# Optimization experiments

Hardware: AMD Instinct MI355X
Metric: run time of the kernel (lower is better)

Reference implementation:

```python
import jax, jax.numpy as jnp
import numpy as np

N_GRAPHS = 256
GRADES = jnp.array([0, 1, 1, 1, 2, 2, 2, 3])      # blade -> grade for Cl(3,0): [1,e1,e2,e3,e12,e13,e23,e123]
G_ONEHOT = jnp.eye(4)[GRADES]                      # (8,4) blade->grade one-hot
NUM_RBF, CUTOFF, NEG_SLOPE = 20, 10.0, 0.2
HID, HEADS, HD, LAYERS = 64, 4, 16, 4
EPS_LN = 1e-6


def _mv_linear_sub(x, w, b):
    # MVLinear with per-grade weights. x:(N,I,8), w:(4,O,I), b:(O,) added to scalar blade.
    wb = w[GRADES]                                 # (8,O,I)
    out = jnp.einsum('nib,boi->nob', x, wb)
    return out.at[..., 0].add(b)


def _gat_layer(h, src, dst, edge_scalar, pw, pb, asrc, adst, wsrc, wdst):
    N = h.shape[0]
    z = _mv_linear_sub(h, pw, pb).reshape(N, HEADS, HD, 8)
    # fold per-grade importance weights into per-blade contraction vectors
    a_s = asrc * wsrc[:, GRADES][:, None, :]       # (H,C,8)
    a_d = adst * wdst[:, GRADES][:, None, :]
    s_src = jnp.einsum('nhcb,hcb->nh', z, a_s)
    s_dst = jnp.einsum('nhcb,hcb->nh', z, a_d)
    e = jax.nn.leaky_relu(s_src[src] + s_dst[dst] + edge_scalar, NEG_SLOPE)  # (E,H)
    e_max = jax.ops.segment_max(e, dst, num_segments=N)
    alpha = jnp.exp(e - e_max[dst])
    a_sum = jax.ops.segment_sum(alpha, dst, num_segments=N)
    alpha = alpha / (a_sum[dst] + 1e-16)
    out = jax.ops.segment_sum(z[src] * alpha[:, :, None, None], dst, num_segments=N)
    return out.reshape(N, HEADS * HD, 8)


def _mv_silu(x, a, b):
    # x:(N,C,8); a,b:(C,4). Gate by scalar part (grade 0) and per-grade squared magnitudes.
    qg = jnp.einsum('ncb,bg->ncg', x * x, G_ONEHOT)                 # (N,C,4) mag2 per grade
    norms = jnp.concatenate([x[..., :1], qg[..., 1:]], axis=-1)     # (N,C,4)
    gate = jax.nn.sigmoid(a * norms + b)[..., GRADES]               # (N,C,8)
    return gate * x


def _mv_layernorm(x, a):
    n = jnp.sqrt(jnp.sum(x * x, axis=-1))                           # (N,C)
    n = jnp.mean(n, axis=1, keepdims=True) + EPS_LN                 # (N,1)
    return a[None, :, None] * x / n[..., None]


def _forward(floats, z, edge_index, batch):
    (pos, atom_w, inw, inb, ew1, eb1, ew2, eb2,
     proj_w, proj_b, a_src, a_dst, w_src, w_dst,
     ln_a, silu_a, silu_b, ppw, ppb, pw1, pb1, pw2, pb2) = floats
    src, dst = edge_index[0], edge_index[1]
    N = pos.shape[0]

    # RBF edge features -> per-head scalar bias
    d2 = jnp.sum((pos[src] - pos[dst]) ** 2, axis=-1)
    dist = jnp.where(d2 > 0, jnp.sqrt(jnp.where(d2 > 0, d2, 1.0)), 0.0)
    centers = jnp.linspace(0.0, CUTOFF, NUM_RBF)
    width = CUTOFF / (NUM_RBF - 1)
    rbf = jnp.exp(-0.5 * ((dist[:, None] - centers) / width) ** 2)  # (E,20)
    edge_scalar = jax.nn.silu(rbf @ ew1.T + eb1) @ ew2.T + eb2      # (E,H)

    # node multivector embedding: scalars from atom embedding, grade-1 from centered positions
    h_sca = jnp.zeros((N, HID, 8), dtype=pos.dtype).at[..., 0].set(atom_w[z])
    cnt = jax.ops.segment_sum(jnp.ones((N,), pos.dtype), batch, num_segments=N_GRAPHS)
    pos_mean = jax.ops.segment_sum(pos, batch, num_segments=N_GRAPHS) / jnp.maximum(cnt, 1.0)[:, None]
    pos_c = pos - pos_mean[batch]
    h_vec = jnp.zeros((N, 1, 8), dtype=pos.dtype).at[:, 0, 1:4].set(pos_c)
    h = jnp.concatenate([h_sca, h_vec], axis=1)                     # (N,HID+1,8)
    h = jnp.einsum('nib,oi->nob', h, inw).at[..., 0].add(inb)       # input_proj, subspaces=False

    for l in range(LAYERS):
        h_res = h
        h = _gat_layer(h, src, dst, edge_scalar, proj_w[l], proj_b[l],
                       a_src[l], a_dst[l], w_src[l], w_dst[l])
        h = _mv_silu(h, silu_a[l], silu_b[l])
        h = h + h_res
        h = _mv_layernorm(h, ln_a[l])

    h = _mv_linear_sub(h, ppw, ppb)[..., 0]                         # (N,HID) scalar blade
    g = jax.ops.segment_sum(h, batch, num_segments=N_GRAPHS)        # 'add' readout -> (B,HID)
    out = jax.nn.silu(g @ pw1.T + pb1) @ pw2.T + pb2                # (B,1)
    return out[:, 0]


def setup_inputs() -> dict:
    key = jax.random.key(0)
    ks = jax.random.split(key, 24)
    N, E, B = 20000, 320000, N_GRAPHS
    rn = lambda k, shape, s=0.1: jax.random.normal(k, shape, jnp.float32) * s
    return dict(
        pos=jax.random.normal(ks[0], (N, 3), jnp.float32) * 3.0,
        z=jax.random.randint(ks[1], (N,), 0, 100),
        edge_index=jax.random.randint(ks[2], (2, E), 0, N),
        batch=jnp.sort(jax.random.randint(ks[3], (N,), 0, B)),
        atom_embed_w=rn(ks[4], (100, HID)),
        inproj_w=rn(ks[5], (HID, HID + 1)),
        inproj_b=rn(ks[6], (HID,)),
        edge_w1=rn(ks[7], (HID, NUM_RBF)),
        edge_b1=rn(ks[8], (HID,)),
        edge_w2=rn(ks[9], (HEADS, HID)),
        edge_b2=rn(ks[10], (HEADS,)),
        proj_w=rn(ks[11], (LAYERS, 4, HID, HID)),
        proj_b=rn(ks[12], (LAYERS, HID)),
        a_src=rn(ks[13], (LAYERS, HEADS, HD, 8)),
        a_dst=rn(ks[14], (LAYERS, HEADS, HD, 8)),
        w_src=jnp.ones((LAYERS, HEADS, 4), jnp.float32),
        w_dst=jnp.ones((LAYERS, HEADS, 4), jnp.float32),
        ln_a=jnp.ones((LAYERS, HID), jnp.float32),
        silu_a=jnp.ones((LAYERS, HID, 4), jnp.float32),
        silu_b=jnp.zeros((LAYERS, HID, 4), jnp.float32),
        prepool_w=rn(ks[15], (4, HID, HID)),
        prepool_b=rn(ks[16], (HID,)),
        post_w1=rn(ks[17], (HID, HID)),
        post_b1=rn(ks[18], (HID,)),
        post_w2=rn(ks[19], (1, HID)),
        post_b2=rn(ks[20], (1,)),
    )


def reference(pos, z, edge_index, batch, atom_embed_w, inproj_w, inproj_b,
              edge_w1, edge_b1, edge_w2, edge_b2, proj_w, proj_b,
              a_src, a_dst, w_src, w_dst, ln_a, silu_a, silu_b,
              prepool_w, prepool_b, post_w1, post_b1, post_w2, post_b2):
    floats = (pos, atom_embed_w, inproj_w, inproj_b, edge_w1, edge_b1, edge_w2, edge_b2,
              proj_w, proj_b, a_src, a_dst, w_src, w_dst,
              ln_a, silu_a, silu_b, prepool_w, prepool_b, post_w1, post_b1, post_w2, post_b2)
    return _forward(floats, z, edge_index, batch)
```

## Files before the change

kernel.cpp:

```cpp
#include <hip/hip_runtime.h>
#include <hip/hip_bf16.h>
#include <math.h>

#define HID 64
#define HEADS 4
#define LAYERS 4
#define NRBF 20
#define NG 256
#define CB 512
#define HSTRIDE 68
#define CAPB 64
#define TABN 8192
#define NATOM 100

typedef __attribute__((ext_vector_type(8))) short short8;
typedef __attribute__((ext_vector_type(4))) float floatx4;

__device__ __forceinline__ int gradeOf(int b){ return (b==0)?0:((b<4)?1:((b<7)?2:3)); }
__device__ __forceinline__ unsigned short f2bf(float f){
    __hip_bfloat16 h = __float2bfloat16(f);
    return *(unsigned short*)&h;
}
__device__ __forceinline__ float bflo(int u){ return __uint_as_float(((unsigned)u)<<16); }
__device__ __forceinline__ float bfhi(int u){ return __uint_as_float(((unsigned)u)&0xFFFF0000u); }
__device__ __forceinline__ int packbf2(float a, float b){
    return (int)f2bf(a) | ((int)f2bf(b)<<16);
}

struct P {
    const float *pos; const int *zidx; const int *ei; const int *batch;
    const float *atom_w, *inproj_w, *inproj_b, *ew1, *eb1, *ew2, *eb2;
    const float *proj_w, *proj_b, *a_src, *a_dst, *w_src, *w_dst;
    const float *ln_a, *silu_a, *silu_b, *ppw, *ppb, *pw1, *pb1, *pw2, *pb2;
    float *out;
    int *counts; float *possum; float *pcnt; float *gbuf;
    int *bucket;
    int *escb;
    float *tab;
    unsigned short *WTbf; float *ppw0T; float *w1T; float *sbf;
    float *embT;
    unsigned short *hb;
    unsigned short *zA; unsigned short *zB;
    float *ssA; float *sdA; float *ssB; float *sdB;
    int N, E, Mtiles;
};

__global__ __launch_bounds__(256) void k1_kernel(P p){
    const int PREP_TOTAL = LAYERS*4*64*64 + 2*HID*HID + 2*LAYERS*HEADS;
    const int CP = (PREP_TOTAL+255)/256;
    const int CG = NG/4;
    const int CT = (TABN+1+3)/4;
    int bid = blockIdx.x, t = threadIdx.x;
    if (bid < CP){
        int idx = bid*256 + t;
        const int szW = LAYERS*4*64*64;
        const int e2 = szW + HID*HID;
        const int e3 = e2 + HID*HID;
        if (idx < szW){
            p.WTbf[idx] = f2bf(p.proj_w[idx]);
        } else if (idx < e2){
            int r = idx - szW; int i = r/HID, o = r%HID;
            p.ppw0T[r] = p.ppw[o*HID + i];
        } else if (idx < e3){
            int r = idx - e2; int i = r/HID, o = r%HID;
            p.w1T[r] = p.pw1[o*HID + i];
        } else if (idx < e3 + 2*LAYERS*HEADS){
            int r = idx - e3;
            int hh = r & 3; int type = (r>>2)&1; int l = r>>3;
            const float* a = type ? p.a_dst : p.a_src;
            const float* w = type ? p.w_dst : p.w_src;
            float wh = w[l*16 + hh*4 + 0];
            float s = 0.f;
            for (int c=0;c<16;c++)
                s += a[l*512 + (hh*16+c)*8 + 0] * wh * p.proj_b[l*64 + hh*16 + c];
            p.sbf[r] = s;
        }
    } else if (bid < CP+CG){
        int wv = t>>6, lane = t&63;
        int g = (bid-CP)*4 + wv;
        int lo = 0, hi = p.N;
        while (lo < hi){ int mid = (lo+hi)>>1; if (p.batch[mid] < g) lo = mid+1; else hi = mid; }
        int s0 = lo;
        hi = p.N;
        while (lo < hi){ int mid = (lo+hi)>>1; if (p.batch[mid] < g+1) lo = mid+1; else hi = mid; }
        int s1 = lo;
        float sx=0.f, sy=0.f, sz=0.f;
        for (int i=s0+lane; i<s1; i+=64){
            sx += p.pos[i*3+0]; sy += p.pos[i*3+1]; sz += p.pos[i*3+2];
        }
        #pragma unroll
        for (int off=1; off<64; off<<=1){
            sx += __shfl_xor(sx,off,64);
            sy += __shfl_xor(sy,off,64);
            sz += __shfl_xor(sz,off,64);
        }
        if (lane==0){
            p.possum[g*3+0]=sx; p.possum[g*3+1]=sy; p.possum[g*3+2]=sz;
            p.pcnt[g] = (float)(s1-s0);
        }
    } else if (bid < CP+CG+CT){
        int wv = t>>6, lane = t&63;
        int i = (bid-CP-CG)*4 + wv;
        if (i > TABN) return;
        float d = (float)i * (16.0f/TABN);
        float t0 = d * (19.0f/10.0f);
        float hv = p.eb1[lane];
        #pragma unroll
        for (int k=0;k<NRBF;k++){
            float a = t0 - (float)k;
            hv += __expf(-0.5f*a*a) * p.ew1[lane*NRBF+k];
        }
        float act = hv/(1.0f+__expf(-hv));
        float p0 = act*p.ew2[0*HID+lane];
        float p1 = act*p.ew2[1*HID+lane];
        float p2 = act*p.ew2[2*HID+lane];
        float p3 = act*p.ew2[3*HID+lane];
        #pragma unroll
        for (int off=1; off<64; off<<=1){
            p0 += __shfl_xor(p0,off,64);
            p1 += __shfl_xor(p1,off,64);
            p2 += __shfl_xor(p2,off,64);
            p3 += __shfl_xor(p3,off,64);
        }
        if (lane==0){
            *(float4*)&p.tab[(size_t)i*4] = make_float4(p0+p.eb2[0], p1+p.eb2[1],
                                                        p2+p.eb2[2], p3+p.eb2[3]);
        }
    } else {
        int wv = t>>6, lane = t&63;
        int za = (bid-CP-CG-CT)*4 + wv;
        if (za >= NATOM) return;
        float accv = p.inproj_b[lane];
        for (int i=0;i<HID;i++)
            accv += p.atom_w[(size_t)za*HID + i] * p.inproj_w[lane*65 + i];
        p.embT[(size_t)za*HID + lane] = accv;
    }
}

__device__ __forceinline__ void proj_core(const P& p, int pl, int n0, int nt, int lane,
        const short8* afr, bool rows16,
        unsigned short* zout, float* ssout, float* sdout){
    const unsigned short* WTl = p.WTbf + (size_t)pl*4*64*64;
    const float* pbl = p.proj_b + pl*HID;
    const float* a_src_l = p.a_src + pl*512;
    const float* a_dst_l = p.a_dst + pl*512;
    const float* w_src_l = p.w_src + pl*16;
    const float* w_dst_l = p.w_dst + pl*16;
    const float* sb_l = p.sbf + pl*8;
    int m = lane&15, quad = lane>>4;
    int o = nt*16 + m;
    float cs[4][2][4];
    float pss[4], psd[4];
    #pragma unroll
    for (int r=0;r<4;r++){ pss[r]=0.f; psd[r]=0.f; }
    #pragma unroll
    for (int bp=0; bp<4; bp++){
        const int b0 = 2*bp, b1 = b0+1;
        const int g0 = gradeOf(b0), g1 = gradeOf(b1);
        const short8 w00 = *(const short8*)(WTl + (g0*64 + o)*64 + quad*8);
        const short8 w01 = *(const short8*)(WTl + (g0*64 + o)*64 + 32 + quad*8);
        short8 w10, w11;
        if (g1==g0){ w10 = w00; w11 = w01; }
        else {
            w10 = *(const short8*)(WTl + (g1*64 + o)*64 + quad*8);
            w11 = *(const short8*)(WTl + (g1*64 + o)*64 + 32 + quad*8);
        }
        floatx4 c0 = {0.f,0.f,0.f,0.f}, c1 = {0.f,0.f,0.f,0.f};
        c0 = __builtin_amdgcn_mfma_f32_16x16x32_bf16(afr[4*bp+0], w00, c0, 0,0,0);
        c0 = __builtin_amdgcn_mfma_f32_16x16x32_bf16(afr[4*bp+1], w01, c0, 0,0,0);
        c1 = __builtin_amdgcn_mfma_f32_16x16x32_bf16(afr[4*bp+2], w10, c1, 0,0,0);
        c1 = __builtin_amdgcn_mfma_f32_16x16x32_bf16(afr[4*bp+3], w11, c1, 0,0,0);
        float as0 = a_src_l[o*8+b0]*w_src_l[nt*4+g0];
        float as1 = a_src_l[o*8+b1]*w_src_l[nt*4+g1];
        float ad0 = a_dst_l[o*8+b0]*w_dst_l[nt*4+g0];
        float ad1 = a_dst_l[o*8+b1]*w_dst_l[nt*4+g1];
        float bias0 = (bp==0) ? pbl[o] : 0.0f;
        #pragma unroll
        for (int r=0;r<4;r++){
            float v0 = c0[r], v1 = c1[r];
            pss[r] += v0*as0 + v1*as1;
            psd[r] += v0*ad0 + v1*ad1;
            cs[bp][0][r] = v0 + bias0;
            cs[bp][1][r] = v1;
        }
    }
    #pragma unroll
    for (int r=0;r<4;r++){
        int row = quad*4 + r;
        bool rowok = rows16 ? true : (quad==0);
        int nn = n0 + (rows16 ? row : r);
        if (rowok && nn < p.N){
            unsigned short pk[8];
            #pragma unroll
            for (int bp=0;bp<4;bp++){
                pk[2*bp]   = f2bf(cs[bp][0][r]);
                pk[2*bp+1] = f2bf(cs[bp][1][r]);
            }
            *(int4*)(zout + (size_t)nn*CB + o*8) = *(int4*)pk;
        }
    }
    #pragma unroll
    for (int r=0;r<4;r++){
        float vs = pss[r], vd = psd[r];
        #pragma unroll
        for (int off=1; off<16; off<<=1){
            vs += __shfl_xor(vs, off, 64);
            vd += __shfl_xor(vd, off, 64);
        }
        int row = quad*4 + r;
        bool rowok = rows16 ? true : (quad==0);
        int nn = n0 + (rows16 ? row : r);
        if (m==0 && rowok && nn<p.N){
            ssout[nn*4+nt] = vs + sb_l[nt];
            sdout[nn*4+nt] = vd + sb_l[4+nt];
        }
    }
}

__global__ __launch_bounds__(256) void k2_kernel(P p){
    __shared__ unsigned short hAl[8*16*HSTRIDE];
    int t = threadIdx.x, wv = t>>6, lane = t&63;
    if ((int)blockIdx.x >= p.Mtiles){
        int e = ((int)blockIdx.x - p.Mtiles)*256 + t;
        if (e >= p.E) return;
        int s = p.ei[e], d = p.ei[p.E+e];
        float dx = p.pos[s*3+0]-p.pos[d*3+0];
        float dy = p.pos[s*3+1]-p.pos[d*3+1];
        float dz = p.pos[s*3+2]-p.pos[d*3+2];
        float dist = sqrtf(dx*dx+dy*dy+dz*dz);
        float idxf = fminf(dist * ((float)TABN/16.0f), (float)(TABN-1));
        int i0 = (int)idxf;
        float fr = idxf - (float)i0;
        float4 f0 = *(const float4*)&p.tab[(size_t)i0*4];
        float4 f1 = *(const float4*)&p.tab[(size_t)(i0+1)*4];
        int slot = atomicAdd(&p.counts[d],1);
        if (slot < CAPB){
            p.bucket[(size_t)d*CAPB + slot] = s;
            int2 epk = make_int2(
                packbf2(f0.x + (f1.x-f0.x)*fr, f0.y + (f1.y-f0.y)*fr),
                packbf2(f0.z + (f1.z-f0.z)*fr, f0.w + (f1.w-f0.w)*fr));
            *(int2*)&p.escb[((size_t)d*CAPB + slot)*2] = epk;
        }
        return;
    }
    int n0 = blockIdx.x*16;
    float wvv = p.inproj_w[lane*65 + 64];
    for (int k=0;k<4;k++){
        int m = wv*4 + k;
        int n = n0 + m;
        if (n < p.N){
            int zn = p.zidx[n];
            float acc = p.embT[(size_t)zn*HID + lane];
            int g = p.batch[n];
            float cm = p.pcnt[g]; cm = cm>1.0f?cm:1.0f;
            float px = p.pos[n*3+0]-p.possum[g*3+0]/cm;
            float py = p.pos[n*3+1]-p.possum[g*3+1]/cm;
            float pz = p.pos[n*3+2]-p.possum[g*3+2]/cm;
            unsigned short pk[8];
            pk[0]=f2bf(acc); pk[1]=f2bf(wvv*px); pk[2]=f2bf(wvv*py); pk[3]=f2bf(wvv*pz);
            pk[4]=0; pk[5]=0; pk[6]=0; pk[7]=0;
            *(int4*)(p.hb + (size_t)n*CB + lane*8) = *(int4*)pk;
            #pragma unroll
            for (int b=0;b<8;b++) hAl[(b*16+m)*HSTRIDE + lane] = pk[b];
        } else {
            #pragma unroll
            for (int b=0;b<8;b++) hAl[(b*16+m)*HSTRIDE + lane] = 0;
        }
    }
    __syncthreads();
    int m = lane&15, quad = lane>>4;
    short8 afr[16];
    #pragma unroll
    for (int bp=0;bp<4;bp++){
        int b0=2*bp, b1=b0+1;
        afr[4*bp+0] = *(const short8*)(hAl + (b0*16+m)*HSTRIDE + quad*8);
        afr[4*bp+1] = *(const short8*)(hAl + (b0*16+m)*HSTRIDE + 32 + quad*8);
        afr[4*bp+2] = *(const short8*)(hAl + (b1*16+m)*HSTRIDE + quad*8);
        afr[4*bp+3] = *(const short8*)(hAl + (b1*16+m)*HSTRIDE + 32 + quad*8);
    }
    proj_core(p, 0, n0, wv, lane, afr, true, p.zA, p.ssA, p.sdA);
}

__device__ __forceinline__ void fmab8(const float* lwv, int h_id, int J,
                                      const int4* zv, float* acc, float& dn){
    #pragma unroll
    for (int i=0;i<8;i++){
        float w = lwv[(J+i)*4 + h_id];
        acc[0] += w*bflo(zv[i].x); acc[1] += w*bfhi(zv[i].x);
        acc[2] += w*bflo(zv[i].y); acc[3] += w*bfhi(zv[i].y);
        acc[4] += w*bflo(zv[i].z); acc[5] += w*bfhi(zv[i].z);
        acc[6] += w*bflo(zv[i].w); acc[7] += w*bfhi(zv[i].w);
        dn += w;
    }
}

__global__ __launch_bounds__(256) void agg_kernel(P p, int l,
        const unsigned short* __restrict__ zin, const float* __restrict__ ssin,
        const float* __restrict__ sdin, int last){
    __shared__ float lw[4][256];
    int wv = threadIdx.x>>6, lane = threadIdx.x&63;
    int n = blockIdx.x*4 + wv;
    if (n >= p.N) return;
    float* lwv = lw[wv];
    int4 hres = *((const int4*)(p.hb + (size_t)n*CB) + lane);
    float4 sdl = *(const float4*)&sdin[n*4];
    int deg = min(p.counts[n], CAPB);
    int h_id = lane>>4;
    const int* bs = p.bucket + (size_t)n*CAPB;
    int s = 0;
    float l0=-1e30f,l1=-1e30f,l2=-1e30f,l3=-1e30f;
    if (lane < deg){
        s = bs[lane];
        int2 ev = *((const int2*)p.escb + ((size_t)n*CAPB + lane));
        float4 sv  = *(const float4*)&ssin[s*4];
        l0 = sv.x+sdl.x+bflo(ev.x); l0=(l0>=0.f)?l0:0.2f*l0;
        l1 = sv.y+sdl.y+bfhi(ev.x); l1=(l1>=0.f)?l1:0.2f*l1;
        l2 = sv.z+sdl.z+bflo(ev.y); l2=(l2>=0.f)?l2:0.2f*l2;
        l3 = sv.w+sdl.w+bfhi(ev.y); l3=(l3>=0.f)?l3:0.2f*l3;
    }
    int bc = (deg+7)>>3;
    int4 zv[8];
    if (bc>0){
        #pragma unroll
        for (int i=0;i<8;i++){
            int sb = __builtin_amdgcn_readlane(s, i);
            zv[i] = *((const int4*)(zin + (size_t)(unsigned)sb*CB) + lane);
        }
    }
    float m0=l0,m1=l1,m2=l2,m3=l3;
    #pragma unroll
    for (int off=1; off<64; off<<=1){
        m0=fmaxf(m0,__shfl_xor(m0,off,64));
        m1=fmaxf(m1,__shfl_xor(m1,off,64));
        m2=fmaxf(m2,__shfl_xor(m2,off,64));
        m3=fmaxf(m3,__shfl_xor(m3,off,64));
    }
    *(float4*)&lwv[lane*4] = make_float4(__expf(l0-m0),__expf(l1-m1),
                                         __expf(l2-m2),__expf(l3-m3));
    float acc[8];
    #pragma unroll
    for (int k=0;k<8;k++) acc[k]=0.f;
    float dn = 0.f;
    if (bc>0) fmab8(lwv, h_id, 0, zv, acc, dn);
    for (int j=8; j<bc*8; j+=8){
        #pragma unroll
        for (int i=0;i<8;i++){
            int sb = __builtin_amdgcn_readlane(s, j+i);
            zv[i] = *((const int4*)(zin + (size_t)(unsigned)sb*CB) + lane);
        }
        fmab8(lwv, h_id, j, zv, acc, dn);
    }
    float inv = 1.0f/(dn + 1e-16f);
    float x[8];
    #pragma unroll
    for (int k=0;k<8;k++) x[k] = acc[k]*inv;
    const float* silu_a_l = p.silu_a + l*HID*4;
    const float* silu_b_l = p.silu_b + l*HID*4;
    float4 sa = *(const float4*)&silu_a_l[lane*4];
    float4 sb = *(const float4*)&silu_b_l[lane*4];
    float n1 = x[1]*x[1]+x[2]*x[2]+x[3]*x[3];
    float n2 = x[4]*x[4]+x[5]*x[5]+x[6]*x[6];
    float n3 = x[7]*x[7];
    float g0 = 1.0f/(1.0f+__expf(-(sa.x*x[0]+sb.x)));
    float g1 = 1.0f/(1.0f+__expf(-(sa.y*n1+sb.y)));
    float g2 = 1.0f/(1.0f+__expf(-(sa.z*n2+sb.z)));
    float g3 = 1.0f/(1.0f+__expf(-(sa.w*n3+sb.w)));
    float val[8];
    val[0]=g0*x[0]+bflo(hres.x); val[1]=g1*x[1]+bfhi(hres.x);
    val[2]=g1*x[2]+bflo(hres.y); val[3]=g1*x[3]+bfhi(hres.y);
    val[4]=g2*x[4]+bflo(hres.z); val[5]=g2*x[5]+bfhi(hres.z);
    val[6]=g2*x[6]+bflo(hres.w); val[7]=g3*x[7]+bfhi(hres.w);
    float ssq=0.f;
    #pragma unroll
    for (int k=0;k<8;k++) ssq += val[k]*val[k];
    float nr = sqrtf(ssq);
    #pragma unroll
    for (int off=1; off<64; off<<=1) nr += __shfl_xor(nr, off, 64);
    float mean = nr*(1.0f/64.0f) + 1e-6f;
    float scale = p.ln_a[l*HID + lane]/mean;
    float outv[8];
    #pragma unroll
    for (int k=0;k<8;k++) outv[k] = scale*val[k];
    if (!last){
        unsigned short pk[8];
        #pragma unroll
        for (int k=0;k<8;k++) pk[k] = f2bf(outv[k]);
        *(int4*)(p.hb + (size_t)n*CB + lane*8) = *(int4*)pk;
    } else {
        atomicAdd(&p.gbuf[p.batch[n]*HID + lane], outv[0]);
    }
}

__global__ __launch_bounds__(512) void proj_kernel(P p, int pl,
        unsigned short* zout, float* ssout, float* sdout){
    __shared__ unsigned short hAl[2][8*16*HSTRIDE];
    int t = threadIdx.x, wv = t>>6, lane = t&63;
    int nb = blockIdx.x*32;
    for (int k=0;k<4;k++){
        int m2 = wv*4 + k;
        int tile = m2>>4, mr = m2&15;
        int n = nb + m2;
        if (n < p.N){
            int4 hv = *((const int4*)(p.hb + (size_t)n*CB) + lane);
            unsigned short* pk = (unsigned short*)&hv;
            #pragma unroll
            for (int b=0;b<8;b++) hAl[tile][(b*16+mr)*HSTRIDE + lane] = pk[b];
        } else {
            #pragma unroll
            for (int b=0;b<8;b++) hAl[tile][(b*16+mr)*HSTRIDE + lane] = 0;
        }
    }
    __syncthreads();
    int tile = wv>>2, nt = wv&3;
    int n0 = nb + tile*16;
    const unsigned short* hT = hAl[tile];
    int m = lane&15, quad = lane>>4;
    short8 afr[16];
    #pragma unroll
    for (int bp=0;bp<4;bp++){
        int b0=2*bp, b1=b0+1;
        afr[4*bp+0] = *(const short8*)(hT + (b0*16+m)*HSTRIDE + quad*8);
        afr[4*bp+1] = *(const short8*)(hT + (b0*16+m)*HSTRIDE + 32 + quad*8);
        afr[4*bp+2] = *(const short8*)(hT + (b1*16+m)*HSTRIDE + quad*8);
        afr[4*bp+3] = *(const short8*)(hT + (b1*16+m)*HSTRIDE + 32 + quad*8);
    }
    proj_core(p, pl, n0, nt, lane, afr, true, zout, ssout, sdout);
}

__global__ void final_kernel(P p){
    int gid = blockIdx.x; int o = threadIdx.x;
    float gs = p.gbuf[gid*HID + o];
    float cnt = p.pcnt[gid];
    float gsc = cnt * p.ppb[o];
    for (int i=0;i<HID;i++) gsc += __shfl(gs, i, 64) * p.ppw0T[i*HID + o];
    float a = p.pb1[o];
    for (int i=0;i<HID;i++) a += __shfl(gsc, i, 64) * p.w1T[i*HID + o];
    float act = a/(1.0f+__expf(-a));
    float pv = act * p.pw2[o];
    #pragma unroll
    for (int off=1; off<64; off<<=1) pv += __shfl_xor(pv, off, 64);
    if (o==0) p.out[gid] = pv + p.pb2[0];
}

extern "C" void kernel_launch(void* const* d_in, const int* in_sizes, int n_in,
                              void* d_out, int out_size, void* d_ws, size_t ws_size,
                              hipStream_t stream) {
    P p;
    p.pos      = (const float*)d_in[0];
    p.zidx     = (const int*)  d_in[1];
    p.ei       = (const int*)  d_in[2];
    p.batch    = (const int*)  d_in[3];
    p.atom_w   = (const float*)d_in[4];
    p.inproj_w = (const float*)d_in[5];
    p.inproj_b = (const float*)d_in[6];
    p.ew1      = (const float*)d_in[7];
    p.eb1      = (const float*)d_in[8];
    p.ew2      = (const float*)d_in[9];
    p.eb2      = (const float*)d_in[10];
    p.proj_w   = (const float*)d_in[11];
    p.proj_b   = (const float*)d_in[12];
    p.a_src    = (const float*)d_in[13];
    p.a_dst    = (const float*)d_in[14];
    p.w_src    = (const float*)d_in[15];
    p.w_dst    = (const float*)d_in[16];
    p.ln_a     = (const float*)d_in[17];
    p.silu_a   = (const float*)d_in[18];
    p.silu_b   = (const float*)d_in[19];
    p.ppw      = (const float*)d_in[20];
    p.ppb      = (const float*)d_in[21];
    p.pw1      = (const float*)d_in[22];
    p.pb1      = (const float*)d_in[23];
    p.pw2      = (const float*)d_in[24];
    p.pb2      = (const float*)d_in[25];
    p.out = (float*)d_out;

    const int N = in_sizes[0]/3;
    const int E = in_sizes[2]/2;
    p.N = N; p.E = E; p.Mtiles = (N+15)/16;

    float* wsf = (float*)d_ws;
    size_t off = 0;
    auto alloc = [&](size_t nelem){ size_t r = off; off += (nelem + 63) & ~(size_t)63; return r; };
    size_t o_counts = alloc(N);
    size_t o_g      = alloc(NG*HID);
    size_t zero_end = off;
    size_t o_possum = alloc(NG*3);
    size_t o_pcnt   = alloc(NG);
    size_t o_bucket = alloc((size_t)N*CAPB);
    size_t o_escb   = alloc((size_t)N*CAPB*2);
    size_t o_tab    = alloc((size_t)(TABN+2)*4);
    size_t o_ssA    = alloc((size_t)N*4);
    size_t o_sdA    = alloc((size_t)N*4);
    size_t o_ssB    = alloc((size_t)N*4);
    size_t o_sdB    = alloc((size_t)N*4);
    size_t o_WTbf   = alloc((size_t)LAYERS*4*64*64/2);
    size_t o_ppw0T  = alloc(HID*HID);
    size_t o_w1T    = alloc(HID*HID);
    size_t o_sbf    = alloc(2*LAYERS*HEADS);
    size_t o_embT   = alloc((size_t)NATOM*HID);
    size_t o_hb     = alloc((size_t)N*CB/2);
    size_t o_zA     = alloc((size_t)N*CB/2);
    size_t o_zB     = alloc((size_t)N*CB/2);

    p.counts = (int*)(wsf + o_counts);
    p.gbuf   = wsf + o_g;
    p.possum = wsf + o_possum;
    p.pcnt   = wsf + o_pcnt;
    p.bucket = (int*)(wsf + o_bucket);
    p.escb   = (int*)(wsf + o_escb);
    p.tab    = wsf + o_tab;
    p.ssA    = wsf + o_ssA;
    p.sdA    = wsf + o_sdA;
    p.ssB    = wsf + o_ssB;
    p.sdB    = wsf + o_sdB;
    p.WTbf   = (unsigned short*)(wsf + o_WTbf);
    p.ppw0T  = wsf + o_ppw0T;
    p.w1T    = wsf + o_w1T;
    p.sbf    = wsf + o_sbf;
    p.embT   = wsf + o_embT;
    p.hb     = (unsigned short*)(wsf + o_hb);
    p.zA     = (unsigned short*)(wsf + o_zA);
    p.zB     = (unsigned short*)(wsf + o_zB);

    hipMemsetAsync(wsf, 0, zero_end*sizeof(float), stream);

    const int PREP_TOTAL = LAYERS*4*64*64 + 2*HID*HID + 2*LAYERS*HEADS;
    const int CP = (PREP_TOTAL+255)/256;
    const int CG = NG/4;
    const int CE = (E+255)/256;
    const int CT = (TABN+1+3)/4;
    const int CEMB = (NATOM+3)/4;

    k1_kernel<<<CP+CG+CT+CEMB, 256, 0, stream>>>(p);
    k2_kernel<<<p.Mtiles + CE, 256, 0, stream>>>(p);

    const int AG = (N+3)/4;
    const int PG = (N+31)/32;
    agg_kernel <<<AG, 256, 0, stream>>>(p, 0, p.zA, p.ssA, p.sdA, 0);
    proj_kernel<<<PG, 512, 0, stream>>>(p, 1, p.zB, p.ssB, p.sdB);
    agg_kernel <<<AG, 256, 0, stream>>>(p, 1, p.zB, p.ssB, p.sdB, 0);
    proj_kernel<<<PG, 512, 0, stream>>>(p, 2, p.zA, p.ssA, p.sdA);
    agg_kernel <<<AG, 256, 0, stream>>>(p, 2, p.zA, p.ssA, p.sdA, 0);
    proj_kernel<<<PG, 512, 0, stream>>>(p, 3, p.zB, p.ssB, p.sdB);
    agg_kernel <<<AG, 256, 0, stream>>>(p, 3, p.zB, p.ssB, p.sdB, 1);

    final_kernel<<<NG, 64, 0, stream>>>(p);
}
```

Measured before the change: 408.2 us.

## Fuse attention aggregation with next-layer projection into one kernel

Merges each layer's agg_kernel with the following proj_kernel. A 1024-thread block aggregates 16 nodes (one wave per node), writes the normalized features into shared memory, and four waves then run the MFMA projection for the next layer. This removes three kernel launches and the separate global re-read of h that the projection kernel did. It also loads the A fragments inside the projection loop instead of preloading all 16, which lowers register pressure. In exchange, the 1024-thread blocks leave 12 of 16 waves idle during projection, and the larger blocks may reduce occupancy.

```diff
diff --git a/kernel.cpp b/kernel.cpp
--- a/kernel.cpp
+++ b/kernel.cpp
@@ -138,7 +138,7 @@
 }
 
 __device__ __forceinline__ void proj_core(const P& p, int pl, int n0, int nt, int lane,
-        const short8* afr, bool rows16,
+        const unsigned short* hAl,
         unsigned short* zout, float* ssout, float* sdout){
     const unsigned short* WTl = p.WTbf + (size_t)pl*4*64*64;
     const float* pbl = p.proj_b + pl*HID;
@@ -157,6 +157,10 @@
     for (int bp=0; bp<4; bp++){
         const int b0 = 2*bp, b1 = b0+1;
         const int g0 = gradeOf(b0), g1 = gradeOf(b1);
+        const short8 a0 = *(const short8*)(hAl + (b0*16+m)*HSTRIDE + quad*8);
+        const short8 a1 = *(const short8*)(hAl + (b0*16+m)*HSTRIDE + 32 + quad*8);
+        const short8 a2 = *(const short8*)(hAl + (b1*16+m)*HSTRIDE + quad*8);
+        const short8 a3 = *(const short8*)(hAl + (b1*16+m)*HSTRIDE + 32 + quad*8);
         const short8 w00 = *(const short8*)(WTl + (g0*64 + o)*64 + quad*8);
         const short8 w01 = *(const short8*)(WTl + (g0*64 + o)*64 + 32 + quad*8);
         short8 w10, w11;
@@ -166,10 +170,10 @@
             w11 = *(const short8*)(WTl + (g1*64 + o)*64 + 32 + quad*8);
         }
         floatx4 c0 = {0.f,0.f,0.f,0.f}, c1 = {0.f,0.f,0.f,0.f};
-        c0 = __builtin_amdgcn_mfma_f32_16x16x32_bf16(afr[4*bp+0], w00, c0, 0,0,0);
-        c0 = __builtin_amdgcn_mfma_f32_16x16x32_bf16(afr[4*bp+1], w01, c0, 0,0,0);
-        c1 = __builtin_amdgcn_mfma_f32_16x16x32_bf16(afr[4*bp+2], w10, c1, 0,0,0);
-        c1 = __builtin_amdgcn_mfma_f32_16x16x32_bf16(afr[4*bp+3], w11, c1, 0,0,0);
+        c0 = __builtin_amdgcn_mfma_f32_16x16x32_bf16(a0, w00, c0, 0,0,0);
+        c0 = __builtin_amdgcn_mfma_f32_16x16x32_bf16(a1, w01, c0, 0,0,0);
+        c1 = __builtin_amdgcn_mfma_f32_16x16x32_bf16(a2, w10, c1, 0,0,0);
+        c1 = __builtin_amdgcn_mfma_f32_16x16x32_bf16(a3, w11, c1, 0,0,0);
         float as0 = a_src_l[o*8+b0]*w_src_l[nt*4+g0];
         float as1 = a_src_l[o*8+b1]*w_src_l[nt*4+g1];
         float ad0 = a_dst_l[o*8+b0]*w_dst_l[nt*4+g0];
@@ -186,10 +190,8 @@
     }
     #pragma unroll
     for (int r=0;r<4;r++){
-        int row = quad*4 + r;
-        bool rowok = rows16 ? true : (quad==0);
-        int nn = n0 + (rows16 ? row : r);
-        if (rowok && nn < p.N){
+        int nn = n0 + quad*4 + r;
+        if (nn < p.N){
             unsigned short pk[8];
             #pragma unroll
             for (int bp=0;bp<4;bp++){
@@ -207,10 +209,8 @@
             vs += __shfl_xor(vs, off, 64);
             vd += __shfl_xor(vd, off, 64);
         }
-        int row = quad*4 + r;
-        bool rowok = rows16 ? true : (quad==0);
-        int nn = n0 + (rows16 ? row : r);
-        if (m==0 && rowok && nn<p.N){
+        int nn = n0 + quad*4 + r;
+        if (m==0 && nn<p.N){
             ssout[nn*4+nt] = vs + sb_l[nt];
             sdout[nn*4+nt] = vd + sb_l[4+nt];
         }
@@ -268,17 +268,7 @@
         }
     }
     __syncthreads();
-    int m = lane&15, quad = lane>>4;
-    short8 afr[16];
-    #pragma unroll
-    for (int bp=0;bp<4;bp++){
-        int b0=2*bp, b1=b0+1;
-        afr[4*bp+0] = *(const short8*)(hAl + (b0*16+m)*HSTRIDE + quad*8);
-        afr[4*bp+1] = *(const short8*)(hAl + (b0*16+m)*HSTRIDE + 32 + quad*8);
-        afr[4*bp+2] = *(const short8*)(hAl + (b1*16+m)*HSTRIDE + quad*8);
-        afr[4*bp+3] = *(const short8*)(hAl + (b1*16+m)*HSTRIDE + 32 + quad*8);
-    }
-    proj_core(p, 0, n0, wv, lane, afr, true, p.zA, p.ssA, p.sdA);
+    proj_core(p, 0, n0, wv, lane, hAl, p.zA, p.ssA, p.sdA);
 }
 
 __device__ __forceinline__ void fmab8(const float* lwv, int h_id, int J,
@@ -294,14 +284,9 @@
     }
 }
 
-__global__ __launch_bounds__(256) void agg_kernel(P p, int l,
+__device__ __forceinline__ void agg_node(const P& p, int l, int n, int lane, float* lwv,
         const unsigned short* __restrict__ zin, const float* __restrict__ ssin,
-        const float* __restrict__ sdin, int last){
-    __shared__ float lw[4][256];
-    int wv = threadIdx.x>>6, lane = threadIdx.x&63;
-    int n = blockIdx.x*4 + wv;
-    if (n >= p.N) return;
-    float* lwv = lw[wv];
+        const float* __restrict__ sdin, float* outv){
     int4 hres = *((const int4*)(p.hb + (size_t)n*CB) + lane);
     float4 sdl = *(const float4*)&sdin[n*4];
     int deg = min(p.counts[n], CAPB);
@@ -378,53 +363,44 @@
     for (int off=1; off<64; off<<=1) nr += __shfl_xor(nr, off, 64);
     float mean = nr*(1.0f/64.0f) + 1e-6f;
     float scale = p.ln_a[l*HID + lane]/mean;
-    float outv[8];
     #pragma unroll
     for (int k=0;k<8;k++) outv[k] = scale*val[k];
-    if (!last){
-        unsigned short pk[8];
+}
+
+__global__ __launch_bounds__(1024) void aggproj_kernel(P p, int l,
+        const unsigned short* __restrict__ zin, const float* __restrict__ ssin,
+        const float* __restrict__ sdin,
+        unsigned short* zout, float* ssout, float* sdout){
+    __shared__ float lw[16][256];
+    __shared__ unsigned short hAl[8*16*HSTRIDE];
+    int wv = threadIdx.x>>6, lane = threadIdx.x&63;
+    int n0 = blockIdx.x*16;
+    int n = n0 + wv;
+    unsigned short pk[8] = {0,0,0,0,0,0,0,0};
+    if (n < p.N){
+        float outv[8];
+        agg_node(p, l, n, lane, lw[wv], zin, ssin, sdin, outv);
         #pragma unroll
         for (int k=0;k<8;k++) pk[k] = f2bf(outv[k]);
         *(int4*)(p.hb + (size_t)n*CB + lane*8) = *(int4*)pk;
-    } else {
-        atomicAdd(&p.gbuf[p.batch[n]*HID + lane], outv[0]);
-    }
-}
-
-__global__ __launch_bounds__(512) void proj_kernel(P p, int pl,
-        unsigned short* zout, float* ssout, float* sdout){
-    __shared__ unsigned short hAl[2][8*16*HSTRIDE];
-    int t = threadIdx.x, wv = t>>6, lane = t&63;
-    int nb = blockIdx.x*32;
-    for (int k=0;k<4;k++){
-        int m2 = wv*4 + k;
-        int tile = m2>>4, mr = m2&15;
-        int n = nb + m2;
-        if (n < p.N){
-            int4 hv = *((const int4*)(p.hb + (size_t)n*CB) + lane);
-            unsigned short* pk = (unsigned short*)&hv;
-            #pragma unroll
-            for (int b=0;b<8;b++) hAl[tile][(b*16+mr)*HSTRIDE + lane] = pk[b];
-        } else {
-            #pragma unroll
-            for (int b=0;b<8;b++) hAl[tile][(b*16+mr)*HSTRIDE + lane] = 0;
-        }
-    }
+    }
+    #pragma unroll
+    for (int b=0;b<8;b++) hAl[(b*16+wv)*HSTRIDE + lane] = pk[b];
     __syncthreads();
-    int tile = wv>>2, nt = wv&3;
-    int n0 = nb + tile*16;
-    const unsigned short* hT = hAl[tile];
-    int m = lane&15, quad = lane>>4;
-    short8 afr[16];
-    #pragma unroll
-    for (int bp=0;bp<4;bp++){
-        int b0=2*bp, b1=b0+1;
-        afr[4*bp+0] = *(const short8*)(hT + (b0*16+m)*HSTRIDE + quad*8);
-        afr[4*bp+1] = *(const short8*)(hT + (b0*16+m)*HSTRIDE + 32 + quad*8);
-        afr[4*bp+2] = *(const short8*)(hT + (b1*16+m)*HSTRIDE + quad*8);
-        afr[4*bp+3] = *(const short8*)(hT + (b1*16+m)*HSTRIDE + 32 + quad*8);
-    }
-    proj_core(p, pl, n0, nt, lane, afr, true, zout, ssout, sdout);
+    if (wv < 4)
+        proj_core(p, l+1, n0, wv, lane, hAl, zout, ssout, sdout);
+}
+
+__global__ __launch_bounds__(256) void agg_kernel(P p, int l,
+        const unsigned short* __restrict__ zin, const float* __restrict__ ssin,
+        const float* __restrict__ sdin){
+    __shared__ float lw[4][256];
+    int wv = threadIdx.x>>6, lane = threadIdx.x&63;
+    int n = blockIdx.x*4 + wv;
+    if (n >= p.N) return;
+    float outv[8];
+    agg_node(p, l, n, lane, lw[wv], zin, ssin, sdin, outv);
+    atomicAdd(&p.gbuf[p.batch[n]*HID + lane], outv[0]);
 }
 
 __global__ void final_kernel(P p){
@@ -534,15 +510,11 @@
     k1_kernel<<<CP+CG+CT+CEMB, 256, 0, stream>>>(p);
     k2_kernel<<<p.Mtiles + CE, 256, 0, stream>>>(p);
 
-    const int AG = (N+3)/4;
-    const int PG = (N+31)/32;
-    agg_kernel <<<AG, 256, 0, stream>>>(p, 0, p.zA, p.ssA, p.sdA, 0);
-    proj_kernel<<<PG, 512, 0, stream>>>(p, 1, p.zB, p.ssB, p.sdB);
-    agg_kernel <<<AG, 256, 0, stream>>>(p, 1, p.zB, p.ssB, p.sdB, 0);
-    proj_kernel<<<PG, 512, 0, stream>>>(p, 2, p.zA, p.ssA, p.sdA);
-    agg_kernel <<<AG, 256, 0, stream>>>(p, 2, p.zA, p.ssA, p.sdA, 0);
-    proj_kernel<<<PG, 512, 0, stream>>>(p, 3, p.zB, p.ssB, p.sdB);
-    agg_kernel <<<AG, 256, 0, stream>>>(p, 3, p.zB, p.ssB, p.sdB, 1);
+    const int FG = (N+15)/16;
+    aggproj_kernel<<<FG, 1024, 0, stream>>>(p, 0, p.zA, p.ssA, p.sdA, p.zB, p.ssB, p.sdB);
+    aggproj_kernel<<<FG, 1024, 0, stream>>>(p, 1, p.zB, p.ssB, p.sdB, p.zA, p.ssA, p.sdA);
+    aggproj_kernel<<<FG, 1024, 0, stream>>>(p, 2, p.zA, p.ssA, p.sdA, p.zB, p.ssB, p.sdB);
+    agg_kernel    <<<(N+3)/4, 256, 0, stream>>>(p, 3, p.zB, p.ssB, p.sdB);
 
     final_kernel<<<NG, 64, 0, stream>>>(p);
 }
```

After: 388.5 us, median of 2. 4.8% less time.
